# Kernel optimization log

Hardware: AMD Instinct MI355X
Metric: run time of the kernel (lower is better)

The kernel has to match this reference:

```python
import jax, jax.numpy as jnp
import numpy as np

B, N, D, H, DFF = 4096, 64, 256, 8, 1024
HD = D // H

def _ln(x, g, b):
    m = jnp.mean(x, axis=-1, keepdims=True)
    v = jnp.var(x, axis=-1, keepdims=True)
    return (x - m) / jnp.sqrt(v + 1e-5) * g + b


def setup_inputs() -> dict:
    key = jax.random.key(0)
    ks = jax.random.split(key, 16)
    s = jnp.float32(0.02)
    def rn(k, shape):
        return jax.random.normal(k, shape, dtype=jnp.float32) * s
    d2 = D // 2
    return {
        "x": jax.random.normal(ks[0], (B, N, 1), dtype=jnp.float32),
        "ve_w1": rn(ks[1], (1, d2)), "ve_b1": jnp.zeros((d2,), jnp.float32),
        "ve_w2": rn(ks[2], (d2, D)), "ve_b2": jnp.zeros((D,), jnp.float32),
        "pos_emb": rn(ks[3], (100, D)),
        "attn_in_w": rn(ks[4], (D, 3 * D)), "attn_in_b": jnp.zeros((3 * D,), jnp.float32),
        "attn_out_w": rn(ks[5], (D, D)), "attn_out_b": jnp.zeros((D,), jnp.float32),
        "ffn_w1": rn(ks[6], (D, DFF)), "ffn_b1": jnp.zeros((DFF,), jnp.float32),
        "ffn_w2": rn(ks[7], (DFF, D)), "ffn_b2": jnp.zeros((D,), jnp.float32),
        "ln1_g": jnp.ones((D,), jnp.float32), "ln1_b": jnp.zeros((D,), jnp.float32),
        "ln2_g": jnp.ones((D,), jnp.float32), "ln2_b": jnp.zeros((D,), jnp.float32),
        "rank_emb": rn(ks[8], (100, D)),
        "q_w": rn(ks[9], (D, D)), "q_b": jnp.zeros((D,), jnp.float32),
        "k_w": rn(ks[10], (D, D)), "k_b": jnp.zeros((D,), jnp.float32),
    }


def reference(x, ve_w1, ve_b1, ve_w2, ve_b2, pos_emb, attn_in_w, attn_in_b,
              attn_out_w, attn_out_b, ffn_w1, ffn_b1, ffn_w2, ffn_b2,
              ln1_g, ln1_b, ln2_g, ln2_b, rank_emb, q_w, q_b, k_w, k_b):
    # ---- encode ----
    v = jax.nn.relu(x @ ve_w1 + ve_b1) @ ve_w2 + ve_b2          # [B,N,D]
    h = v + pos_emb[:N][None]                                    # broadcast pos embed
    qkv = h @ attn_in_w + attn_in_b
    q, k, vv = jnp.split(qkv, 3, axis=-1)
    split_heads = lambda t: t.reshape(B, N, H, HD).transpose(0, 2, 1, 3)
    q, k, vv = split_heads(q), split_heads(k), split_heads(vv)
    scores = jnp.einsum('bhqd,bhkd->bhqk', q, k) / jnp.sqrt(jnp.float32(HD))
    attn = jax.nn.softmax(scores, axis=-1)
    ao = jnp.einsum('bhqk,bhkd->bhqd', attn, vv).transpose(0, 2, 1, 3).reshape(B, N, D)
    ao = ao @ attn_out_w + attn_out_b
    h = _ln(h + ao, ln1_g, ln1_b)
    ff = jax.nn.relu(h @ ffn_w1 + ffn_b1) @ ffn_w2 + ffn_b2
    enc = _ln(h + ff, ln2_g, ln2_b)                              # [B,N,D]

    # ---- pointer decode (greedy, coverage mask) ----
    Q = rank_emb[:N] @ q_w + q_b                                 # [N,D] rank queries
    K = enc @ k_w + k_b                                          # [B,N,D]
    base = jnp.einsum('td,bnd->tbn', Q, K)                       # [N,B,N] unmasked logits per rank
    bidx = jnp.arange(B)

    def step(mask, base_t):
        logits_t = jnp.where(mask > 0, base_t, -jnp.inf)         # masked_fill
        chosen = jnp.argmax(logits_t, axis=-1)                   # greedy pick
        mask = mask.at[bidx, chosen].set(0.0)                    # scatter mask update
        return mask, logits_t

    mask0 = jnp.ones((B, N), jnp.float32)
    _, all_logits = jax.lax.scan(step, mask0, base)              # [N,B,N]
    return all_logits.transpose(1, 0, 2)                         # [B,N,N]
```

## Files before the change

### kernel.cpp

```cpp
#include <hip/hip_runtime.h>
#include <math.h>


typedef __attribute__((ext_vector_type(8))) short bf16x8;
typedef __attribute__((ext_vector_type(4))) float f32x4;

#define NEG_FILL (-3.0e38f)

#define U_Q    0
#define U_VE   2048
#define U_QKV  6144
#define U_WO   30720
#define U_F1   38912
#define U_F2   71680
#define U_KW   104448
#define U_TOT  112640

#define SH_H  0
#define SH_A  16384
#define SH_SHORTS 32768
#define FB_FLOATS 4096
#define LDS_BYTES (SH_SHORTS*2 + FB_FLOATS*4)

__device__ __forceinline__ unsigned short f2bf(float f){
  unsigned u = __float_as_uint(f);
  return (unsigned short)((u + 0x7FFFu + ((u>>16)&1u)) >> 16);
}
__device__ __forceinline__ unsigned short f2bt(float f){
  return (unsigned short)(__float_as_uint(f) >> 16);
}
__device__ __forceinline__ float bf2f(unsigned short h){
  return __uint_as_float(((unsigned)h) << 16);
}

#define MFMA(a,b,c) __builtin_amdgcn_mfma_f32_16x16x32_bf16((a),(b),(c),0,0,0)
#define SM_SCALE 0.17677669529663687f

__global__ void __launch_bounds__(256) prep_q(const float* __restrict__ rank_emb,
                                              const float* __restrict__ q_w,
                                              const float* __restrict__ q_b,
                                              short* __restrict__ wsp) {
    int t = blockIdx.x;
    int c = threadIdx.x;
    float acc = q_b[c];
    for (int d = 0; d < 256; d += 4) {
        acc += rank_emb[t*256 + d + 0] * q_w[(d+0)*256 + c]
             + rank_emb[t*256 + d + 1] * q_w[(d+1)*256 + c]
             + rank_emb[t*256 + d + 2] * q_w[(d+2)*256 + c]
             + rank_emb[t*256 + d + 3] * q_w[(d+3)*256 + c];
    }
    int kb = c >> 5, lane = ((c>>3)&3)*16 + (t&15), j = c & 7;
    int u = ((t>>4)*8 + kb)*64 + lane;
    wsp[(U_Q + u)*8 + j] = (short)f2bf(acc);
}

__global__ void __launch_bounds__(256) prep_w(const float* __restrict__ ve_w2,
                                              const float* __restrict__ attn_in_w,
                                              const float* __restrict__ attn_out_w,
                                              const float* __restrict__ ffn_w1,
                                              const float* __restrict__ ffn_w2,
                                              const float* __restrict__ k_w,
                                              short* __restrict__ wsp) {
    int r = blockIdx.x*256 + threadIdx.x;
    const float* w; int N, K, base;
    if (r < 4096)                { w = ve_w2;      N = 256;  K = 128;  base = U_VE;  }
    else if ((r -= 4096)  < 24576) { w = attn_in_w;  N = 768;  K = 256;  base = U_QKV; }
    else if ((r -= 24576) < 8192)  { w = attn_out_w; N = 256;  K = 256;  base = U_WO;  }
    else if ((r -= 8192)  < 32768) { w = ffn_w1;     N = 1024; K = 256;  base = U_F1;  }
    else if ((r -= 32768) < 32768) { w = ffn_w2;     N = 256;  K = 1024; base = U_F2;  }
    else     { r -= 32768;           w = k_w;        N = 256;  K = 256;  base = U_KW;  }
    int KB = K >> 5;
    int lane = r & 63;
    int kb   = (r >> 6) % KB;
    int nt   = r / (64 * KB);
    int n  = nt*16 + (lane & 15);
    int k0 = kb*32 + (lane >> 4)*8;
    bf16x8 hv;
#pragma unroll
    for (int j = 0; j < 8; j++) hv[j] = (short)f2bf(w[(size_t)(k0 + j)*N + n]);
    *(bf16x8*)&wsp[(size_t)(base + r) * 8] = hv;
}

__global__ void __launch_bounds__(512, 4) fused_kernel(
    const float* __restrict__ x,
    const float* __restrict__ ve_w1, const float* __restrict__ ve_b1,
    const float* __restrict__ ve_b2,
    const float* __restrict__ pos_emb,
    const float* __restrict__ attn_in_b,
    const float* __restrict__ attn_out_b,
    const float* __restrict__ ffn_b1, const float* __restrict__ ffn_b2,
    const float* __restrict__ ln1_g, const float* __restrict__ ln1_b,
    const float* __restrict__ ln2_g, const float* __restrict__ ln2_b,
    const float* __restrict__ k_b,
    const short* __restrict__ wsp,
    float* __restrict__ out)
{
    extern __shared__ short sm[];
    float* smf  = (float*)(sm + SH_SHORTS);
    float* SB   = smf;

    const int tid  = threadIdx.x;
    const int b    = blockIdx.x;
    const int w    = tid >> 6;
    const int lane = tid & 63;
    const int quad = lane >> 4;
    const int lcol = lane & 15;

    const bf16x8* wsv = (const bf16x8*)wsp;
    const bf16x8* HFu = (const bf16x8*)&sm[SH_H];
    bf16x8* HFw = (bf16x8*)&sm[SH_H];

#pragma unroll
    for (int i = 0; i < 2; i++) {
        int u = tid + i*512;
        int l3 = u & 63, kb = (u >> 6) & 3, mt = u >> 8;
        int m  = mt*16 + (l3 & 15);
        int k0 = kb*32 + (l3 >> 4)*8;
        float xv = x[b*64 + m];
        bf16x8 hv;
#pragma unroll
        for (int j = 0; j < 8; j++) {
            float f = xv * ve_w1[k0 + j] + ve_b1[k0 + j];
            hv[j] = (short)f2bt(f > 0.f ? f : 0.f);
        }
        *(bf16x8*)&sm[SH_A + u*8] = hv;
    }
    __syncthreads();

    {
        f32x4 acc[2][4];
#pragma unroll
        for (int s = 0; s < 2; s++)
#pragma unroll
            for (int mi = 0; mi < 4; mi++) acc[s][mi] = (f32x4){0.f,0.f,0.f,0.f};
#pragma unroll
        for (int kb = 0; kb < 4; kb++) {
            bf16x8 bh0 = wsv[U_VE + ((w    )*4+kb)*64 + lane];
            bf16x8 bh1 = wsv[U_VE + ((w + 8)*4+kb)*64 + lane];
#pragma unroll
            for (int mi = 0; mi < 4; mi++) {
                bf16x8 ah = *(const bf16x8*)&sm[SH_A + ((mi*4+kb)*64 + lane)*8];
                acc[0][mi] = MFMA(ah, bh0, acc[0][mi]);
                acc[1][mi] = MFMA(ah, bh1, acc[1][mi]);
            }
        }
        __syncthreads();
#pragma unroll
        for (int s = 0; s < 2; s++) {
            int n = (w + s*8)*16 + lcol;
#pragma unroll
            for (int mi = 0; mi < 4; mi++)
#pragma unroll
                for (int reg = 0; reg < 4; reg++) {
                    int m = mi*16 + quad*4 + reg;
                    float val = acc[s][mi][reg] + ve_b2[n] + pos_emb[m*256 + n];
                    int kb2 = n >> 5, l2 = ((n>>3)&3)*16 + (m&15), j2 = n & 7;
                    sm[SH_H + ((mi*8 + kb2)*64 + l2)*8 + j2] = (short)f2bt(val);
                }
        }
    }
    __syncthreads();

    f32x4 aoacc[2][4];
#pragma unroll
    for (int s = 0; s < 2; s++)
#pragma unroll
        for (int mi = 0; mi < 4; mi++) aoacc[s][mi] = (f32x4){0.f,0.f,0.f,0.f};

    const int il = w & 3;
    const int eo = il >> 1, ch = il & 1;

    auto qkv_phase = [&](int p) {
        int ntv = 32 + 4*p + il;
        if (w < 4) {
            int ntg = 4*p + il;
            f32x4 acc[4];
#pragma unroll
            for (int mi = 0; mi < 4; mi++) acc[mi] = (f32x4){0.f,0.f,0.f,0.f};
#pragma unroll
            for (int kb = 0; kb < 8; kb++) {
                bf16x8 bh = wsv[U_QKV + (ntg*8+kb)*64 + lane];
#pragma unroll
                for (int mi = 0; mi < 4; mi++)
                    acc[mi] = MFMA(HFu[(mi*8+kb)*64 + lane], bh, acc[mi]);
            }
#pragma unroll
            for (int mi = 0; mi < 4; mi++)
#pragma unroll
                for (int reg = 0; reg < 4; reg++) {
                    int m  = mi*16 + quad*4 + reg;
                    int cc = ch*16 + lcol;
                    short hv = (short)f2bt(acc[mi][reg] + attn_in_b[ntg*16 + lcol]);
                    int l2 = ((cc>>3)&3)*16 + (m&15), j2 = cc & 7;
                    sm[SH_A + eo*2048 + (mi*64 + l2)*8 + j2] = hv;
                }
            f32x4 va[2];
            va[0] = (f32x4){0.f,0.f,0.f,0.f}; va[1] = (f32x4){0.f,0.f,0.f,0.f};
#pragma unroll
            for (int kb = 0; kb < 8; kb++) {
                bf16x8 bh = wsv[U_QKV + (ntv*8+kb)*64 + lane];
                va[0] = MFMA(HFu[(0*8+kb)*64 + lane], bh, va[0]);
                va[1] = MFMA(HFu[(1*8+kb)*64 + lane], bh, va[1]);
            }
#pragma unroll
            for (int mi = 0; mi < 2; mi++)
#pragma unroll
                for (int reg = 0; reg < 4; reg++) {
                    int m  = mi*16 + quad*4 + reg;
                    int cc = ch*16 + lcol;
                    short hv = (short)f2bt(va[mi][reg] + attn_in_b[ntv*16 + lcol]);
                    int kb2 = m >> 5;
                    int l2 = ((m>>3)&3)*16 + lcol, j2 = m & 7;
                    sm[SH_A + 8192 + eo*2048 + ((ch*2 + kb2)*64 + l2)*8 + j2] = hv;
                }
        } else {
            int ntg = 16 + 4*p + il;
            f32x4 acc[4];
#pragma unroll
            for (int mi = 0; mi < 4; mi++) acc[mi] = (f32x4){0.f,0.f,0.f,0.f};
#pragma unroll
            for (int kb = 0; kb < 8; kb++) {
                bf16x8 bh = wsv[U_QKV + (ntg*8+kb)*64 + lane];
#pragma unroll
                for (int mi = 0; mi < 4; mi++)
                    acc[mi] = MFMA(HFu[(mi*8+kb)*64 + lane], bh, acc[mi]);
            }
#pragma unroll
            for (int mi = 0; mi < 4; mi++)
#pragma unroll
                for (int reg = 0; reg < 4; reg++) {
                    int m  = mi*16 + quad*4 + reg;
                    int cc = ch*16 + lcol;
                    short hv = (short)f2bt(acc[mi][reg] + attn_in_b[ntg*16 + lcol]);
                    int l2 = ((cc>>3)&3)*16 + (m&15), j2 = cc & 7;
                    sm[SH_A + 4096 + eo*2048 + ((m>>4)*64 + l2)*8 + j2] = hv;
                }
            f32x4 va[2];
            va[0] = (f32x4){0.f,0.f,0.f,0.f}; va[1] = (f32x4){0.f,0.f,0.f,0.f};
#pragma unroll
            for (int kb = 0; kb < 8; kb++) {
                bf16x8 bh = wsv[U_QKV + (ntv*8+kb)*64 + lane];
                va[0] = MFMA(HFu[(2*8+kb)*64 + lane], bh, va[0]);
                va[1] = MFMA(HFu[(3*8+kb)*64 + lane], bh, va[1]);
            }
#pragma unroll
            for (int mi2 = 0; mi2 < 2; mi2++)
#pragma unroll
                for (int reg = 0; reg < 4; reg++) {
                    int m  = (mi2+2)*16 + quad*4 + reg;
                    int cc = ch*16 + lcol;
                    short hv = (short)f2bt(va[mi2][reg] + attn_in_b[ntv*16 + lcol]);
                    int kb2 = m >> 5;
                    int l2 = ((m>>3)&3)*16 + lcol, j2 = m & 7;
                    sm[SH_A + 8192 + eo*2048 + ((ch*2 + kb2)*64 + l2)*8 + j2] = hv;
                }
        }
    };

    auto scores_sm = [&](int e) {
        if (w < 4) {
            int mi = w;
            bf16x8 ah = *(const bf16x8*)&sm[SH_A + e*2048 + (mi*64 + lane)*8];
            f32x4 sa[4];
#pragma unroll
            for (int ni = 0; ni < 4; ni++) {
                bf16x8 bh = *(const bf16x8*)&sm[SH_A + 4096 + e*2048 + (ni*64 + lane)*8];
                f32x4 z = (f32x4){0.f,0.f,0.f,0.f};
                sa[ni] = MFMA(ah, bh, z);
            }
#pragma unroll
            for (int reg = 0; reg < 4; reg++) {
                float v0 = sa[0][reg]*SM_SCALE, v1 = sa[1][reg]*SM_SCALE;
                float v2 = sa[2][reg]*SM_SCALE, v3 = sa[3][reg]*SM_SCALE;
                float mx = fmaxf(fmaxf(v0,v1), fmaxf(v2,v3));
#pragma unroll
                for (int off = 8; off >= 1; off >>= 1) mx = fmaxf(mx, __shfl_xor(mx, off, 64));
                v0 = __expf(v0-mx); v1 = __expf(v1-mx); v2 = __expf(v2-mx); v3 = __expf(v3-mx);
                float s = v0+v1+v2+v3;
#pragma unroll
                for (int off = 8; off >= 1; off >>= 1) s += __shfl_xor(s, off, 64);
                float inv = 1.0f / s;
                float pr[4] = {v0*inv, v1*inv, v2*inv, v3*inv};
                int mr = quad*4 + reg;
#pragma unroll
                for (int ni = 0; ni < 4; ni++) {
                    int u  = mi*2 + (ni>>1);
                    int l2 = ((ni*2 + (lcol>>3))&3)*16 + mr;
                    sm[SH_SHORTS + e*4096 + u*512 + l2*8 + (lcol&7)] = (short)f2bt(pr[ni]);
                }
            }
        }
    };

    auto pv_phase = [&](int e) {
        int mi = w & 3, ni = w >> 2;
        f32x4 pv = (f32x4){0.f,0.f,0.f,0.f};
#pragma unroll
        for (int kb = 0; kb < 2; kb++) {
            bf16x8 ah = *(const bf16x8*)&sm[SH_SHORTS + e*4096 + ((mi*2+kb)*64 + lane)*8];
            bf16x8 bh = *(const bf16x8*)&sm[SH_A + 8192 + e*2048 + ((ni*2+kb)*64 + lane)*8];
            pv = MFMA(ah, bh, pv);
        }
#pragma unroll
        for (int reg = 0; reg < 4; reg++) {
            int m = mi*16 + quad*4 + reg;
            int c = ni*16 + lcol;
            int l2 = ((c>>3)&3)*16 + (m&15), j2 = c & 7;
            sm[SH_A + 12288 + e*2048 + (mi*64 + l2)*8 + j2] = (short)f2bt(pv[reg]);
        }
    };

    auto wo_phase = [&](int hh, int e) {
        bf16x8 bh0 = wsv[U_WO + ((w    )*8 + hh)*64 + lane];
        bf16x8 bh1 = wsv[U_WO + ((w + 8)*8 + hh)*64 + lane];
#pragma unroll
        for (int mi = 0; mi < 4; mi++) {
            bf16x8 ah = *(const bf16x8*)&sm[SH_A + 12288 + e*2048 + (mi*64 + lane)*8];
            aoacc[0][mi] = MFMA(ah, bh0, aoacc[0][mi]);
            aoacc[1][mi] = MFMA(ah, bh1, aoacc[1][mi]);
        }
    };

    qkv_phase(0);
    __syncthreads();
    for (int p = 0; p < 4; p++) {
        scores_sm(0);
        __syncthreads();
        pv_phase(0);  scores_sm(1);
        __syncthreads();
        wo_phase(2*p, 0);  pv_phase(1);
        __syncthreads();
        wo_phase(2*p+1, 1);
        if (p < 3) qkv_phase(p+1);
        __syncthreads();
    }

#pragma unroll
    for (int s = 0; s < 2; s++) {
        int n = (w + s*8)*16 + lcol;
#pragma unroll
        for (int mi = 0; mi < 4; mi++)
#pragma unroll
            for (int reg = 0; reg < 4; reg++) {
                int m  = mi*16 + quad*4 + reg;
                int kb2 = n >> 5, l2 = ((n>>3)&3)*16 + (m&15), j2 = n & 7;
                int uu = ((mi*8 + kb2)*64 + l2)*8 + j2;
                float val = bf2f((unsigned short)sm[SH_H + uu]) + aoacc[s][mi][reg] + attn_out_b[n];
                sm[SH_H + uu] = (short)f2bt(val);
            }
    }
    __syncthreads();

    auto layernormFO = [&](const float* __restrict__ g, const float* __restrict__ bt) {
        int m = tid >> 3, kb = tid & 7;
        int ub = ((m>>4)*8 + kb)*64 + (m&15);
        bf16x8 h0 = HFu[ub +  0];
        bf16x8 h1 = HFu[ub + 16];
        bf16x8 h2 = HFu[ub + 32];
        bf16x8 h3 = HFu[ub + 48];
        float v[32];
#pragma unroll
        for (int j = 0; j < 8; j++) {
            v[j]    = bf2f((unsigned short)h0[j]);
            v[8+j]  = bf2f((unsigned short)h1[j]);
            v[16+j] = bf2f((unsigned short)h2[j]);
            v[24+j] = bf2f((unsigned short)h3[j]);
        }
        float sum = 0.f;
#pragma unroll
        for (int i = 0; i < 32; i++) sum += v[i];
#pragma unroll
        for (int off = 4; off >= 1; off >>= 1) sum += __shfl_xor(sum, off, 64);
        float mean = sum * (1.0f/256.0f);
        float s2 = 0.f;
#pragma unroll
        for (int i = 0; i < 32; i++) { float d = v[i] - mean; s2 += d*d; }
#pragma unroll
        for (int off = 4; off >= 1; off >>= 1) s2 += __shfl_xor(s2, off, 64);
        float r = 1.0f / sqrtf(s2 * (1.0f/256.0f) + 1e-5f);
#pragma unroll
        for (int q = 0; q < 4; q++) {
            bf16x8 oh;
#pragma unroll
            for (int j = 0; j < 8; j++) {
                int k = kb*32 + q*8 + j;
                oh[j] = (short)f2bt((v[q*8+j] - mean) * r * g[k] + bt[k]);
            }
            HFw[ub + q*16] = oh;
        }
        __syncthreads();
    };
    layernormFO(ln1_g, ln1_b);

    f32x4 f2acc[2][4];
#pragma unroll
    for (int s = 0; s < 2; s++)
#pragma unroll
        for (int mi = 0; mi < 4; mi++) f2acc[s][mi] = (f32x4){0.f,0.f,0.f,0.f};

    for (int c = 0; c < 4; c++) {
        f32x4 a1[4];
#pragma unroll
        for (int mi = 0; mi < 4; mi++) a1[mi] = (f32x4){0.f,0.f,0.f,0.f};
#pragma unroll
        for (int kb = 0; kb < 8; kb++) {
            bf16x8 bh = wsv[U_F1 + ((c*16 + w)*8 + kb)*64 + lane];
#pragma unroll
            for (int mi = 0; mi < 4; mi++) {
                bf16x8 ah = HFu[(mi*8+kb)*64 + lane];
                a1[mi] = MFMA(ah, bh, a1[mi]);
            }
        }
        __syncthreads();
#pragma unroll
        for (int mi = 0; mi < 4; mi++)
#pragma unroll
            for (int reg = 0; reg < 4; reg++) {
                int m = mi*16 + quad*4 + reg;
                int n = (c*16 + w)*16 + lcol;
                float val = a1[mi][reg] + ffn_b1[n];
                val = val > 0.f ? val : 0.f;
                int kk = w*16 + lcol;
                int kb2 = kk >> 5, l2 = ((kk>>3)&3)*16 + (m&15), j2 = kk & 7;
                sm[SH_A + ((mi*8 + kb2)*64 + l2)*8 + j2] = (short)f2bt(val);
            }
#pragma unroll
        for (int mi = 0; mi < 4; mi++) a1[mi] = (f32x4){0.f,0.f,0.f,0.f};
#pragma unroll
        for (int kb = 0; kb < 8; kb++) {
            bf16x8 bh = wsv[U_F1 + ((c*16 + w + 8)*8 + kb)*64 + lane];
#pragma unroll
            for (int mi = 0; mi < 4; mi++) {
                bf16x8 ah = HFu[(mi*8+kb)*64 + lane];
                a1[mi] = MFMA(ah, bh, a1[mi]);
            }
        }
#pragma unroll
        for (int mi = 0; mi < 4; mi++)
#pragma unroll
            for (int reg = 0; reg < 4; reg++) {
                int m = mi*16 + quad*4 + reg;
                int n = (c*16 + w + 8)*16 + lcol;
                float val = a1[mi][reg] + ffn_b1[n];
                val = val > 0.f ? val : 0.f;
                int kk = (w + 8)*16 + lcol;
                int kb2 = kk >> 5, l2 = ((kk>>3)&3)*16 + (m&15), j2 = kk & 7;
                sm[SH_A + ((mi*8 + kb2)*64 + l2)*8 + j2] = (short)f2bt(val);
            }
        __syncthreads();
#pragma unroll 2
        for (int kbl = 0; kbl < 8; kbl++) {
            bf16x8 bh0 = wsv[U_F2 + ((w    )*32 + c*8 + kbl)*64 + lane];
            bf16x8 bh1 = wsv[U_F2 + ((w + 8)*32 + c*8 + kbl)*64 + lane];
#pragma unroll
            for (int mi = 0; mi < 4; mi++) {
                bf16x8 ah = *(const bf16x8*)&sm[SH_A + ((mi*8+kbl)*64 + lane)*8];
                f2acc[0][mi] = MFMA(ah, bh0, f2acc[0][mi]);
                f2acc[1][mi] = MFMA(ah, bh1, f2acc[1][mi]);
            }
        }
    }
    __syncthreads();
#pragma unroll
    for (int s = 0; s < 2; s++) {
        int n = (w + s*8)*16 + lcol;
#pragma unroll
        for (int mi = 0; mi < 4; mi++)
#pragma unroll
            for (int reg = 0; reg < 4; reg++) {
                int m  = mi*16 + quad*4 + reg;
                int kb2 = n >> 5, l2 = ((n>>3)&3)*16 + (m&15), j2 = n & 7;
                int uu = ((mi*8 + kb2)*64 + l2)*8 + j2;
                float val = bf2f((unsigned short)sm[SH_H + uu]) + f2acc[s][mi][reg] + ffn_b2[n];
                sm[SH_H + uu] = (short)f2bt(val);
            }
    }
    __syncthreads();
    layernormFO(ln2_g, ln2_b);

    {
        f32x4 kacc[2][4];
#pragma unroll
        for (int s = 0; s < 2; s++)
#pragma unroll
            for (int mi = 0; mi < 4; mi++) kacc[s][mi] = (f32x4){0.f,0.f,0.f,0.f};
#pragma unroll
        for (int kb = 0; kb < 8; kb++) {
            bf16x8 bh0 = wsv[U_KW + ((w    )*8+kb)*64 + lane];
            bf16x8 bh1 = wsv[U_KW + ((w + 8)*8+kb)*64 + lane];
#pragma unroll
            for (int mi = 0; mi < 4; mi++) {
                bf16x8 ah = HFu[(mi*8+kb)*64 + lane];
                kacc[0][mi] = MFMA(ah, bh0, kacc[0][mi]);
                kacc[1][mi] = MFMA(ah, bh1, kacc[1][mi]);
            }
        }
        __syncthreads();
#pragma unroll
        for (int s = 0; s < 2; s++) {
            int n = (w + s*8)*16 + lcol;
#pragma unroll
            for (int mi = 0; mi < 4; mi++)
#pragma unroll
                for (int reg = 0; reg < 4; reg++) {
                    int m = mi*16 + quad*4 + reg;
                    int nt2 = m >> 4, kb2 = n >> 5;
                    int l2 = ((n>>3)&3)*16 + (m&15), j2 = n & 7;
                    sm[SH_H + ((nt2*8 + kb2)*64 + l2)*8 + j2] =
                        (short)f2bt(kacc[s][mi][reg] + k_b[n]);
                }
        }
    }
    __syncthreads();

#pragma unroll
    for (int it = 0; it < 2; it++) {
        int t = w*2 + it;
        int mi = t >> 2, nt = t & 3;
        f32x4 sacc = (f32x4){0.f,0.f,0.f,0.f};
#pragma unroll
        for (int kb = 0; kb < 8; kb++) {
            bf16x8 bh = HFu[(nt*8+kb)*64 + lane];
            bf16x8 ah = wsv[U_Q + (mi*8+kb)*64 + lane];
            sacc = MFMA(ah, bh, sacc);
        }
#pragma unroll
        for (int reg = 0; reg < 4; reg++) {
            int tt = mi*16 + quad*4 + reg;
            int n = nt*16 + lcol;
            SB[tt*64 + (n ^ ((tt&7)<<2))] = sacc[reg];
        }
    }
    __syncthreads();

    if (tid < 64) {
        int ln = tid;
        bool alive = true;
        float* outb = out + (size_t)b * (64*64);
        for (int t = 0; t < 64; t++) {
            float v  = SB[t*64 + (ln ^ ((t&7)<<2))];
            float lv = alive ? v : NEG_FILL;
            outb[t*64 + ln] = lv;
            float bv = lv;
#pragma unroll
            for (int off = 32; off >= 1; off >>= 1)
                bv = fmaxf(bv, __shfl_xor(bv, off, 64));
            unsigned long long mk = __ballot(lv == bv);
            int bi = __ffsll(mk) - 1;
            if (bi == ln) alive = false;
        }
    }
}

extern "C" void kernel_launch(void* const* d_in, const int* in_sizes, int n_in,
                              void* d_out, int out_size, void* d_ws, size_t ws_size,
                              hipStream_t stream) {
    (void)in_sizes; (void)n_in; (void)out_size; (void)ws_size;
    const float* x          = (const float*)d_in[0];
    const float* ve_w1      = (const float*)d_in[1];
    const float* ve_b1      = (const float*)d_in[2];
    const float* ve_w2      = (const float*)d_in[3];
    const float* ve_b2      = (const float*)d_in[4];
    const float* pos_emb    = (const float*)d_in[5];
    const float* attn_in_w  = (const float*)d_in[6];
    const float* attn_in_b  = (const float*)d_in[7];
    const float* attn_out_w = (const float*)d_in[8];
    const float* attn_out_b = (const float*)d_in[9];
    const float* ffn_w1     = (const float*)d_in[10];
    const float* ffn_b1     = (const float*)d_in[11];
    const float* ffn_w2     = (const float*)d_in[12];
    const float* ffn_b2     = (const float*)d_in[13];
    const float* ln1_g      = (const float*)d_in[14];
    const float* ln1_b      = (const float*)d_in[15];
    const float* ln2_g      = (const float*)d_in[16];
    const float* ln2_b      = (const float*)d_in[17];
    const float* rank_emb   = (const float*)d_in[18];
    const float* q_w        = (const float*)d_in[19];
    const float* q_b        = (const float*)d_in[20];
    const float* k_w        = (const float*)d_in[21];
    const float* k_b        = (const float*)d_in[22];
    float* outp = (float*)d_out;
    short* wsp  = (short*)d_ws;

    (void)hipFuncSetAttribute((const void*)fused_kernel,
                              hipFuncAttributeMaxDynamicSharedMemorySize,
                              (int)LDS_BYTES);

    hipLaunchKernelGGL(prep_q, dim3(64), dim3(256), 0, stream, rank_emb, q_w, q_b, wsp);
    hipLaunchKernelGGL(prep_w, dim3(432), dim3(256), 0, stream,
                       ve_w2, attn_in_w, attn_out_w, ffn_w1, ffn_w2, k_w, wsp);
    hipLaunchKernelGGL(fused_kernel, dim3(4096), dim3(512), LDS_BYTES, stream,
                       x, ve_w1, ve_b1, ve_b2, pos_emb,
                       attn_in_b, attn_out_b,
                       ffn_b1, ffn_b2,
                       ln1_g, ln1_b, ln2_g, ln2_b,
                       k_b, (const short*)wsp, outp);
}
```

Measured before the change: 916.3 us.

## Raise wave priority around MFMA loops and rebalance attention phase schedule

Wraps every MFMA inner loop in s_setprio high/low so that waves issuing matrix work get scheduling priority over waves doing epilogue or memory work. It also restructures the per-head attention loop: all 8 waves now compute scores and softmax for both heads at once instead of 4 waves per head staggered across barriers, then both PV products, then both Wo products. This removes one barrier per iteration and the idle waves in the scores phase, but drops the previous software-pipelined overlap between heads.

After: 857.8 us. 1.07x faster.

```diff
diff --git a/kernel.cpp b/kernel.cpp
--- a/kernel.cpp
+++ b/kernel.cpp
@@ -35,6 +35,8 @@
 
 #define MFMA(a,b,c) __builtin_amdgcn_mfma_f32_16x16x32_bf16((a),(b),(c),0,0,0)
 #define SM_SCALE 0.17677669529663687f
+#define PRIO_HI() __builtin_amdgcn_s_setprio(1)
+#define PRIO_LO() __builtin_amdgcn_s_setprio(0)
 
 __global__ void __launch_bounds__(256) prep_q(const float* __restrict__ rank_emb,
                                               const float* __restrict__ q_w,
@@ -133,6 +135,7 @@
         for (int s = 0; s < 2; s++)
 #pragma unroll
             for (int mi = 0; mi < 4; mi++) acc[s][mi] = (f32x4){0.f,0.f,0.f,0.f};
+        PRIO_HI();
 #pragma unroll
         for (int kb = 0; kb < 4; kb++) {
             bf16x8 bh0 = wsv[U_VE + ((w    )*4+kb)*64 + lane];
@@ -144,6 +147,7 @@
                 acc[1][mi] = MFMA(ah, bh1, acc[1][mi]);
             }
         }
+        PRIO_LO();
         __syncthreads();
 #pragma unroll
         for (int s = 0; s < 2; s++) {
@@ -177,6 +181,7 @@
             f32x4 acc[4];
 #pragma unroll
             for (int mi = 0; mi < 4; mi++) acc[mi] = (f32x4){0.f,0.f,0.f,0.f};
+            PRIO_HI();
 #pragma unroll
             for (int kb = 0; kb < 8; kb++) {
                 bf16x8 bh = wsv[U_QKV + (ntg*8+kb)*64 + lane];
@@ -184,6 +189,7 @@
                 for (int mi = 0; mi < 4; mi++)
                     acc[mi] = MFMA(HFu[(mi*8+kb)*64 + lane], bh, acc[mi]);
             }
+            PRIO_LO();
 #pragma unroll
             for (int mi = 0; mi < 4; mi++)
 #pragma unroll
@@ -196,12 +202,14 @@
                 }
             f32x4 va[2];
             va[0] = (f32x4){0.f,0.f,0.f,0.f}; va[1] = (f32x4){0.f,0.f,0.f,0.f};
+            PRIO_HI();
 #pragma unroll
             for (int kb = 0; kb < 8; kb++) {
                 bf16x8 bh = wsv[U_QKV + (ntv*8+kb)*64 + lane];
                 va[0] = MFMA(HFu[(0*8+kb)*64 + lane], bh, va[0]);
                 va[1] = MFMA(HFu[(1*8+kb)*64 + lane], bh, va[1]);
             }
+            PRIO_LO();
 #pragma unroll
             for (int mi = 0; mi < 2; mi++)
 #pragma unroll
@@ -218,6 +226,7 @@
             f32x4 acc[4];
 #pragma unroll
             for (int mi = 0; mi < 4; mi++) acc[mi] = (f32x4){0.f,0.f,0.f,0.f};
+            PRIO_HI();
 #pragma unroll
             for (int kb = 0; kb < 8; kb++) {
                 bf16x8 bh = wsv[U_QKV + (ntg*8+kb)*64 + lane];
@@ -225,6 +234,7 @@
                 for (int mi = 0; mi < 4; mi++)
                     acc[mi] = MFMA(HFu[(mi*8+kb)*64 + lane], bh, acc[mi]);
             }
+            PRIO_LO();
 #pragma unroll
             for (int mi = 0; mi < 4; mi++)
 #pragma unroll
@@ -237,12 +247,14 @@
                 }
             f32x4 va[2];
             va[0] = (f32x4){0.f,0.f,0.f,0.f}; va[1] = (f32x4){0.f,0.f,0.f,0.f};
+            PRIO_HI();
 #pragma unroll
             for (int kb = 0; kb < 8; kb++) {
                 bf16x8 bh = wsv[U_QKV + (ntv*8+kb)*64 + lane];
                 va[0] = MFMA(HFu[(2*8+kb)*64 + lane], bh, va[0]);
                 va[1] = MFMA(HFu[(3*8+kb)*64 + lane], bh, va[1]);
             }
+            PRIO_LO();
 #pragma unroll
             for (int mi2 = 0; mi2 < 2; mi2++)
 #pragma unroll
@@ -257,37 +269,37 @@
         }
     };
 
-    auto scores_sm = [&](int e) {
-        if (w < 4) {
-            int mi = w;
-            bf16x8 ah = *(const bf16x8*)&sm[SH_A + e*2048 + (mi*64 + lane)*8];
-            f32x4 sa[4];
+    auto scores_sm2 = [&]() {
+        int e = w >> 2, mi = w & 3;
+        bf16x8 ah = *(const bf16x8*)&sm[SH_A + e*2048 + (mi*64 + lane)*8];
+        f32x4 sa[4];
+        PRIO_HI();
+#pragma unroll
+        for (int ni = 0; ni < 4; ni++) {
+            bf16x8 bh = *(const bf16x8*)&sm[SH_A + 4096 + e*2048 + (ni*64 + lane)*8];
+            f32x4 z = (f32x4){0.f,0.f,0.f,0.f};
+            sa[ni] = MFMA(ah, bh, z);
+        }
+        PRIO_LO();
+#pragma unroll
+        for (int reg = 0; reg < 4; reg++) {
+            float v0 = sa[0][reg]*SM_SCALE, v1 = sa[1][reg]*SM_SCALE;
+            float v2 = sa[2][reg]*SM_SCALE, v3 = sa[3][reg]*SM_SCALE;
+            float mx = fmaxf(fmaxf(v0,v1), fmaxf(v2,v3));
+#pragma unroll
+            for (int off = 8; off >= 1; off >>= 1) mx = fmaxf(mx, __shfl_xor(mx, off, 64));
+            v0 = __expf(v0-mx); v1 = __expf(v1-mx); v2 = __expf(v2-mx); v3 = __expf(v3-mx);
+            float s = v0+v1+v2+v3;
+#pragma unroll
+            for (int off = 8; off >= 1; off >>= 1) s += __shfl_xor(s, off, 64);
+            float inv = 1.0f / s;
+            float pr[4] = {v0*inv, v1*inv, v2*inv, v3*inv};
+            int mr = quad*4 + reg;
 #pragma unroll
             for (int ni = 0; ni < 4; ni++) {
-                bf16x8 bh = *(const bf16x8*)&sm[SH_A + 4096 + e*2048 + (ni*64 + lane)*8];
-                f32x4 z = (f32x4){0.f,0.f,0.f,0.f};
-                sa[ni] = MFMA(ah, bh, z);
-            }
-#pragma unroll
-            for (int reg = 0; reg < 4; reg++) {
-                float v0 = sa[0][reg]*SM_SCALE, v1 = sa[1][reg]*SM_SCALE;
-                float v2 = sa[2][reg]*SM_SCALE, v3 = sa[3][reg]*SM_SCALE;
-                float mx = fmaxf(fmaxf(v0,v1), fmaxf(v2,v3));
-#pragma unroll
-                for (int off = 8; off >= 1; off >>= 1) mx = fmaxf(mx, __shfl_xor(mx, off, 64));
-                v0 = __expf(v0-mx); v1 = __expf(v1-mx); v2 = __expf(v2-mx); v3 = __expf(v3-mx);
-                float s = v0+v1+v2+v3;
-#pragma unroll
-                for (int off = 8; off >= 1; off >>= 1) s += __shfl_xor(s, off, 64);
-                float inv = 1.0f / s;
-                float pr[4] = {v0*inv, v1*inv, v2*inv, v3*inv};
-                int mr = quad*4 + reg;
-#pragma unroll
-                for (int ni = 0; ni < 4; ni++) {
-                    int u  = mi*2 + (ni>>1);
-                    int l2 = ((ni*2 + (lcol>>3))&3)*16 + mr;
-                    sm[SH_SHORTS + e*4096 + u*512 + l2*8 + (lcol&7)] = (short)f2bt(pr[ni]);
-                }
+                int u  = mi*2 + (ni>>1);
+                int l2 = ((ni*2 + (lcol>>3))&3)*16 + mr;
+                sm[SH_SHORTS + e*4096 + u*512 + l2*8 + (lcol&7)] = (short)f2bt(pr[ni]);
             }
         }
     };
@@ -295,12 +307,14 @@
     auto pv_phase = [&](int e) {
         int mi = w & 3, ni = w >> 2;
         f32x4 pv = (f32x4){0.f,0.f,0.f,0.f};
+        PRIO_HI();
 #pragma unroll
         for (int kb = 0; kb < 2; kb++) {
             bf16x8 ah = *(const bf16x8*)&sm[SH_SHORTS + e*4096 + ((mi*2+kb)*64 + lane)*8];
             bf16x8 bh = *(const bf16x8*)&sm[SH_A + 8192 + e*2048 + ((ni*2+kb)*64 + lane)*8];
             pv = MFMA(ah, bh, pv);
         }
+        PRIO_LO();
 #pragma unroll
         for (int reg = 0; reg < 4; reg++) {
             int m = mi*16 + quad*4 + reg;
@@ -313,24 +327,24 @@
     auto wo_phase = [&](int hh, int e) {
         bf16x8 bh0 = wsv[U_WO + ((w    )*8 + hh)*64 + lane];
         bf16x8 bh1 = wsv[U_WO + ((w + 8)*8 + hh)*64 + lane];
+        PRIO_HI();
 #pragma unroll
         for (int mi = 0; mi < 4; mi++) {
             bf16x8 ah = *(const bf16x8*)&sm[SH_A + 12288 + e*2048 + (mi*64 + lane)*8];
             aoacc[0][mi] = MFMA(ah, bh0, aoacc[0][mi]);
             aoacc[1][mi] = MFMA(ah, bh1, aoacc[1][mi]);
         }
+        PRIO_LO();
     };
 
     qkv_phase(0);
     __syncthreads();
     for (int p = 0; p < 4; p++) {
-        scores_sm(0);
-        __syncthreads();
-        pv_phase(0);  scores_sm(1);
-        __syncthreads();
-        wo_phase(2*p, 0);  pv_phase(1);
-        __syncthreads();
-        wo_phase(2*p+1, 1);
+        scores_sm2();
+        __syncthreads();
+        pv_phase(0);  pv_phase(1);
+        __syncthreads();
+        wo_phase(2*p, 0);  wo_phase(2*p+1, 1);
         if (p < 3) qkv_phase(p+1);
         __syncthreads();
     }
@@ -402,6 +416,7 @@
         f32x4 a1[4];
 #pragma unroll
         for (int mi = 0; mi < 4; mi++) a1[mi] = (f32x4){0.f,0.f,0.f,0.f};
+        PRIO_HI();
 #pragma unroll
         for (int kb = 0; kb < 8; kb++) {
             bf16x8 bh = wsv[U_F1 + ((c*16 + w)*8 + kb)*64 + lane];
@@ -411,6 +426,7 @@
                 a1[mi] = MFMA(ah, bh, a1[mi]);
             }
         }
+        PRIO_LO();
         __syncthreads();
 #pragma unroll
         for (int mi = 0; mi < 4; mi++)
@@ -426,6 +442,7 @@
             }
 #pragma unroll
         for (int mi = 0; mi < 4; mi++) a1[mi] = (f32x4){0.f,0.f,0.f,0.f};
+        PRIO_HI();
 #pragma unroll
         for (int kb = 0; kb < 8; kb++) {
             bf16x8 bh = wsv[U_F1 + ((c*16 + w + 8)*8 + kb)*64 + lane];
@@ -435,6 +452,7 @@
                 a1[mi] = MFMA(ah, bh, a1[mi]);
             }
         }
+        PRIO_LO();
 #pragma unroll
         for (int mi = 0; mi < 4; mi++)
 #pragma unroll
@@ -448,6 +466,7 @@
                 sm[SH_A + ((mi*8 + kb2)*64 + l2)*8 + j2] = (short)f2bt(val);
             }
         __syncthreads();
+        PRIO_HI();
 #pragma unroll 2
         for (int kbl = 0; kbl < 8; kbl++) {
             bf16x8 bh0 = wsv[U_F2 + ((w    )*32 + c*8 + kbl)*64 + lane];
@@ -459,6 +478,7 @@
                 f2acc[1][mi] = MFMA(ah, bh1, f2acc[1][mi]);
             }
         }
+        PRIO_LO();
     }
     __syncthreads();
 #pragma unroll
@@ -484,6 +504,7 @@
         for (int s = 0; s < 2; s++)
 #pragma unroll
             for (int mi = 0; mi < 4; mi++) kacc[s][mi] = (f32x4){0.f,0.f,0.f,0.f};
+        PRIO_HI();
 #pragma unroll
         for (int kb = 0; kb < 8; kb++) {
             bf16x8 bh0 = wsv[U_KW + ((w    )*8+kb)*64 + lane];
@@ -495,6 +516,7 @@
                 kacc[1][mi] = MFMA(ah, bh1, kacc[1][mi]);
             }
         }
+        PRIO_LO();
         __syncthreads();
 #pragma unroll
         for (int s = 0; s < 2; s++) {
@@ -518,12 +540,14 @@
         int t = w*2 + it;
         int mi = t >> 2, nt = t & 3;
         f32x4 sacc = (f32x4){0.f,0.f,0.f,0.f};
+        PRIO_HI();
 #pragma unroll
         for (int kb = 0; kb < 8; kb++) {
             bf16x8 bh = HFu[(nt*8+kb)*64 + lane];
             bf16x8 ah = wsv[U_Q + (mi*8+kb)*64 + lane];
             sacc = MFMA(ah, bh, sacc);
         }
+        PRIO_LO();
 #pragma unroll
         for (int reg = 0; reg < 4; reg++) {
             int tt = mi*16 + quad*4 + reg;
```
